# Optimization experiments

Hardware: AMD Instinct MI355X
Metric: run time of the kernel (lower is better)

## Reference

```python
import jax, jax.numpy as jnp
import numpy as np

LN_EPS = 1e-12


def setup_inputs() -> dict:
    key = jax.random.key(0)
    k1, k2, k3, k4 = jax.random.split(key, 4)
    B, H, L, D = 2, 12, 2048, 64
    q = jax.random.normal(k1, (B, H, L, D), dtype=jnp.float32)
    k = jax.random.normal(k2, (B, H, L, D), dtype=jnp.float32)
    v = jax.random.normal(k3, (B, H, L, D), dtype=jnp.float32)
    mask = jax.random.randint(k4, (1, 1, L, L), 0, 2).astype(jnp.int32)
    gamma = jnp.ones((D,), dtype=jnp.float32)
    beta = jnp.zeros((D,), dtype=jnp.float32)
    return {"q": q, "k": k, "v": v, "mask": mask, "gamma": gamma, "beta": beta}


def reference(q, k, v, mask, gamma, beta):
    # score = q @ k^T  -> [B, H, L, L]
    score = jnp.einsum("bhqd,bhkd->bhqk", q, k)
    # masked_fill(mask == 0, -10000)
    score = jnp.where(mask == 0, jnp.float32(-10000.0), score)
    # result = score @ v -> [B, H, L, D]  (no softmax)
    result = jnp.einsum("bhqk,bhkd->bhqd", score, v)
    # layer norm over the last dim (d_tensor)
    mean = jnp.mean(result, axis=-1, keepdims=True)
    var = jnp.var(result, axis=-1, keepdims=True)
    normed = (result - mean) / jnp.sqrt(var + LN_EPS)
    return normed * gamma + beta
```

## Files before the change

### kernel.cpp

```cpp
#include <hip/hip_runtime.h>

#define SEQ 2048
#define HD 64
#define NBH 24

#define MB_OFF   0
#define MB_BYTES (32 * 32 * 512)
#define QB_OFF   (MB_OFF + MB_BYTES)
#define QK_BYTES (NBH * SEQ * HD * 2)
#define KB_OFF   (QB_OFF + QK_BYTES)
#define VT_OFF   (KB_OFF + QK_BYTES)
#define WS_NEED  ((size_t)(VT_OFF + QK_BYTES))

typedef __bf16 bfrag8 __attribute__((ext_vector_type(8)));
typedef __bf16 bf16x4 __attribute__((ext_vector_type(4)));
typedef float  floatx4 __attribute__((ext_vector_type(4)));
typedef float  floatx16 __attribute__((ext_vector_type(16)));

__device__ __forceinline__ floatx4 mfma_16x16x32(bfrag8 a, bfrag8 b, floatx4 c) {
    return __builtin_amdgcn_mfma_f32_16x16x32_bf16(a, b, c, 0, 0, 0);
}
__device__ __forceinline__ floatx16 mfma_32x32x16(bfrag8 a, bfrag8 b, floatx16 c) {
    return __builtin_amdgcn_mfma_f32_32x32x16_bf16(a, b, c, 0, 0, 0);
}
__device__ __forceinline__ void gld16(const unsigned char* g, unsigned char* l) {
    __builtin_amdgcn_global_load_lds(
        (const __attribute__((address_space(1))) unsigned int*)g,
        (__attribute__((address_space(3))) unsigned int*)l, 16, 0, 0);
}

__global__ __launch_bounds__(256)
void prep_kernel(const float* __restrict__ qp, const float* __restrict__ kp,
                 const float* __restrict__ vp, const int* __restrict__ maskp,
                 unsigned char* __restrict__ ws)
{
    __shared__ __attribute__((aligned(16))) unsigned char parena[64 * 68 * 4];
    const int t = threadIdx.x;
    const int b = blockIdx.x;

    if (b < 1536) {
        int gt  = b * 256 + t;
        int row = gt >> 3;
        int c   = gt & 7;
        const floatx4* qs = (const floatx4*)(qp + row * 64 + c * 8);
        const floatx4* ks = (const floatx4*)(kp + row * 64 + c * 8);
        floatx4 q0 = qs[0], q1 = qs[1];
        floatx4 k0 = ks[0], k1 = ks[1];
        bfrag8 qpk, kpk;
        #pragma unroll
        for (int i = 0; i < 4; ++i) {
            qpk[i] = (__bf16)q0[i]; qpk[4 + i] = (__bf16)q1[i];
            kpk[i] = (__bf16)k0[i]; kpk[4 + i] = (__bf16)k1[i];
        }
        *(bfrag8*)(ws + QB_OFF + row * 128 + c * 16) = qpk;
        *(bfrag8*)(ws + KB_OFF + row * 128 + ((c ^ (row & 7)) * 16)) = kpk;
    } else if (b < 2304) {
        int bb = b - 1536, bh = bb >> 5, kt = bb & 31;
        float* lf = (float*)parena;
        const floatx4* vg = (const floatx4*)(vp + (bh * SEQ + kt * 64) * 64);
        #pragma unroll
        for (int it = 0; it < 4; ++it) {
            int f = t + it * 256;
            int r = f >> 4, c4 = f & 15;
            floatx4 val = vg[f];
            #pragma unroll
            for (int i = 0; i < 4; ++i) lf[r * 68 + c4 * 4 + i] = val[i];
        }
        __syncthreads();
        int d = t >> 2, kseg = t & 3;
        unsigned char* tb = ws + VT_OFF + (size_t)(bh * 32 + kt) * 8192 + d * 128;
        #pragma unroll
        for (int jj = 0; jj < 2; ++jj) {
            bfrag8 pk;
            #pragma unroll
            for (int e = 0; e < 8; ++e)
                pk[e] = (__bf16)lf[(kseg * 16 + jj * 8 + e) * 68 + d];
            *(bfrag8*)(tb + (((kseg * 2 + jj) ^ (d & 7)) * 16)) = pk;
        }
    } else {
        int cc = b - 2304, qtb = cc >> 5, kt = cc & 31;
        const int w = t >> 6, lane = t & 63;
        #pragma unroll
        for (int it = 0; it < 16; ++it) {
            int rr = it * 4 + w;
            unsigned long long bl = __ballot(maskp[(qtb * 64 + rr) * SEQ + kt * 64 + lane] != 0);
            if (lane == 0)
                *(unsigned long long*)(ws + MB_OFF + (size_t)((qtb * 32 + kt) * 64 + rr) * 8) = bl;
        }
    }
}

__global__ __launch_bounds__(128, 2)
void normattn_main(const unsigned char* __restrict__ ws,
                   const float* __restrict__ gammap, const float* __restrict__ betap,
                   float* __restrict__ outp)
{
    __shared__ __attribute__((aligned(16))) unsigned char sm[32768];

    const int tid  = threadIdx.x;
    const int w    = tid >> 6;
    const int lane = tid & 63;
    const int l32  = lane & 31;
    const int hi   = lane >> 5;

    const int id   = blockIdx.x;
    const int xcd  = id & 7;
    const int s    = id >> 3;
    const int bh   = xcd * 3 + (s >> 5);
    const int qtb  = s & 31;
    const int q0   = qtb * 64;

    unsigned char* slotK = sm + w * 16384;
    unsigned char* slotV = slotK + 8192;

    const unsigned char* gKt = ws + KB_OFF + (size_t)(bh * SEQ) * 128;
    const unsigned char* gVt = ws + VT_OFF + (size_t)(bh * 32) * 8192;
    const unsigned char* gMb = ws + MB_OFF + (size_t)(qtb * 32) * 512;

    bfrag8 qb[2][4];
    #pragma unroll
    for (int qh = 0; qh < 2; ++qh)
        #pragma unroll
        for (int dstep = 0; dstep < 4; ++dstep)
            qb[qh][dstep] = *(const bfrag8*)(ws + QB_OFF +
                (size_t)(bh * SEQ + q0 + qh * 32 + l32) * 128 + dstep * 32 + hi * 16);

    floatx16 acc[2][2];
    #pragma unroll
    for (int i = 0; i < 4; ++i) acc[i >> 1][i & 1] = (floatx16)0.0f;

    auto stage = [&](int kt) {
        const unsigned char* gk = gKt + (size_t)kt * 8192 + lane * 16;
        const unsigned char* gv = gVt + (size_t)kt * 8192 + lane * 16;
        #pragma unroll
        for (int c = 0; c < 8; ++c) {
            gld16(gk + c * 1024, slotK + c * 1024);
            gld16(gv + c * 1024, slotV + c * 1024);
        }
    };
    unsigned long long mnx0, mnx1;
    auto loadmask = [&](int kt) {
        mnx0 = *(const unsigned long long*)(gMb + (size_t)kt * 512 + l32 * 8);
        mnx1 = *(const unsigned long long*)(gMb + (size_t)kt * 512 + 256 + l32 * 8);
    };

    stage(w);
    loadmask(w);

    for (int i = 0; i < 16; ++i) {
        const int kt = w + 2 * i;
        asm volatile("s_waitcnt vmcnt(0)" ::: "memory");
        const unsigned long long mr0 = mnx0, mr1 = mnx1;

        bfrag8 ka[2][4], va[2][2][2];
        #pragma unroll
        for (int kh = 0; kh < 2; ++kh)
            #pragma unroll
            for (int d = 0; d < 4; ++d)
                ka[kh][d] = *(const bfrag8*)(slotK + (kh * 32 + l32) * 128 +
                                             (((d * 2 + hi) ^ (l32 & 7)) << 4));
        #pragma unroll
        for (int dh = 0; dh < 2; ++dh)
            #pragma unroll
            for (int kh = 0; kh < 2; ++kh)
                #pragma unroll
                for (int ks = 0; ks < 2; ++ks)
                    va[dh][kh][ks] = *(const bfrag8*)(slotV + (dh * 32 + l32) * 128 +
                                                      (((kh * 4 + ks * 2 + hi) ^ (l32 & 7)) << 4));
        asm volatile("s_waitcnt lgkmcnt(0)" ::: "memory");
        if (i < 15) { stage(kt + 2); loadmask(kt + 2); }

        #pragma unroll
        for (int kh = 0; kh < 2; ++kh) {
            floatx16 st0 = (floatx16)0.0f, st1 = (floatx16)0.0f;
            #pragma unroll
            for (int d = 0; d < 4; ++d) {
                st0 = mfma_32x32x16(ka[kh][d], qb[0][d], st0);
                st1 = mfma_32x32x16(ka[kh][d], qb[1][d], st1);
            }
            #pragma unroll
            for (int qh = 0; qh < 2; ++qh) {
                const floatx16 st = qh ? st1 : st0;
                const unsigned long long mrow = qh ? mr1 : mr0;
                const unsigned bits = (unsigned)(mrow >> (kh * 32 + 4 * hi));
                unsigned u[8];
                #pragma unroll
                for (int j = 0; j < 8; ++j) {
                    const int kl0 = 2 * (j & 1) + 8 * (j >> 1);
                    float a = ((bits >> kl0) & 1u) ? st[2 * j] : -10000.0f;
                    float b = ((bits >> (kl0 + 1)) & 1u) ? st[2 * j + 1] : -10000.0f;
                    asm("v_cvt_pk_bf16_f32 %0, %1, %2" : "=v"(u[j]) : "v"(a), "v"(b));
                }
                asm("v_permlane32_swap_b32 %0, %1" : "+v"(u[0]), "+v"(u[2]));
                asm("v_permlane32_swap_b32 %0, %1" : "+v"(u[1]), "+v"(u[3]));
                asm("v_permlane32_swap_b32 %0, %1" : "+v"(u[4]), "+v"(u[6]));
                asm("v_permlane32_swap_b32 %0, %1" : "+v"(u[5]), "+v"(u[7]));
                union { unsigned int w4[4]; bfrag8 f; } c0, c1;
                c0.w4[0] = u[0]; c0.w4[1] = u[1]; c0.w4[2] = u[2]; c0.w4[3] = u[3];
                c1.w4[0] = u[4]; c1.w4[1] = u[5]; c1.w4[2] = u[6]; c1.w4[3] = u[7];

                acc[qh][0] = mfma_32x32x16(va[0][kh][0], c0.f, acc[qh][0]);
                acc[qh][0] = mfma_32x32x16(va[0][kh][1], c1.f, acc[qh][0]);
                acc[qh][1] = mfma_32x32x16(va[1][kh][0], c0.f, acc[qh][1]);
                acc[qh][1] = mfma_32x32x16(va[1][kh][1], c1.f, acc[qh][1]);
            }
        }
    }

    unsigned char* ex = sm + 16384;
    if (w == 1) {
        #pragma unroll
        for (int qh = 0; qh < 2; ++qh)
            #pragma unroll
            for (int dh = 0; dh < 2; ++dh)
                #pragma unroll
                for (int jj = 0; jj < 4; ++jj) {
                    floatx4 t;
                    #pragma unroll
                    for (int e = 0; e < 4; ++e) t[e] = acc[qh][dh][jj * 4 + e];
                    *(floatx4*)(ex + (qh * 2 + dh) * 4096 + jj * 1024 + lane * 16) = t;
                }
    }
    __syncthreads();
    if (w == 0) {
        #pragma unroll
        for (int qh = 0; qh < 2; ++qh)
            #pragma unroll
            for (int dh = 0; dh < 2; ++dh)
                #pragma unroll
                for (int jj = 0; jj < 4; ++jj) {
                    floatx4 t = *(const floatx4*)(ex + (qh * 2 + dh) * 4096 + jj * 1024 + lane * 16);
                    #pragma unroll
                    for (int e = 0; e < 4; ++e) acc[qh][dh][jj * 4 + e] += t[e];
                }
        #pragma unroll
        for (int qh = 0; qh < 2; ++qh) {
            float ss = 0.0f, ss2 = 0.0f;
            #pragma unroll
            for (int dh = 0; dh < 2; ++dh)
                #pragma unroll
                for (int r = 0; r < 16; ++r) { float x = acc[qh][dh][r]; ss += x; ss2 += x * x; }
            ss  += __shfl_xor(ss, 32);
            ss2 += __shfl_xor(ss2, 32);
            float mean = ss * (1.0f / 64.0f);
            float var  = ss2 * (1.0f / 64.0f) - mean * mean;
            float rstd = rsqrtf(var + 1e-12f);
            float* orow = outp + (size_t)(bh * SEQ + q0 + qh * 32 + l32) * 64;
            #pragma unroll
            for (int dh = 0; dh < 2; ++dh)
                #pragma unroll
                for (int jj = 0; jj < 4; ++jj) {
                    const int d0 = dh * 32 + jj * 8 + 4 * hi;
                    floatx4 gg = *(const floatx4*)(gammap + d0);
                    floatx4 bb = *(const floatx4*)(betap + d0);
                    floatx4 o;
                    #pragma unroll
                    for (int e = 0; e < 4; ++e)
                        o[e] = (acc[qh][dh][jj * 4 + e] - mean) * rstd * gg[e] + bb[e];
                    *(floatx4*)(orow + d0) = o;
                }
        }
    }
}

#define KROW 72
#define SROW 40
__global__ __launch_bounds__(256, 4)
void normattn_fallback(const float* __restrict__ qp, const float* __restrict__ kp,
                       const float* __restrict__ vp, const int* __restrict__ maskp,
                       const float* __restrict__ gammap, const float* __restrict__ betap,
                       float* __restrict__ outp)
{
    __shared__ __attribute__((aligned(16))) __bf16 sQ[64 * KROW];
    __shared__ __attribute__((aligned(16))) __bf16 sK[64 * KROW];
    __shared__ __attribute__((aligned(16))) __bf16 sV[64 * KROW];
    __shared__ __attribute__((aligned(16))) __bf16 sS[4][16 * SROW];
    __shared__ __attribute__((aligned(8)))  unsigned int sMw[64][2];

    const int tid = threadIdx.x, wave = tid >> 6, lane = tid & 63;
    const int quad = lane >> 4, l16 = lane & 15;
    const int q0 = blockIdx.x * 64, bh = blockIdx.y;
    const int base = bh * SEQ * HD;
    {
        const floatx4* qg = (const floatx4*)(qp + base + q0 * HD);
        #pragma unroll
        for (int it = 0; it < 4; ++it) {
            int idx = tid + it * 256, r = idx >> 4, c = idx & 15;
            floatx4 val = qg[idx];
            bf16x4 pk = {(__bf16)val[0], (__bf16)val[1], (__bf16)val[2], (__bf16)val[3]};
            *(bf16x4*)&sQ[r * KROW + c * 4] = pk;
        }
    }
    __syncthreads();
    bfrag8 qa0 = *(const bfrag8*)&sQ[(wave * 16 + l16) * KROW + quad * 8];
    bfrag8 qa1 = *(const bfrag8*)&sQ[(wave * 16 + l16) * KROW + quad * 8 + 32];
    floatx4 acc[4];
    #pragma unroll
    for (int i = 0; i < 4; ++i) acc[i] = (floatx4)0.0f;
    const int qrow_loc = wave * 16 + quad * 4;
    const int qrb = q0 + qrow_loc;
    for (int kb = 0; kb < SEQ; kb += 64) {
        __syncthreads();
        {
            const floatx4* kg = (const floatx4*)(kp + base + kb * HD);
            #pragma unroll
            for (int it = 0; it < 4; ++it) {
                int idx = tid + it * 256, r = idx >> 4, c = idx & 15;
                floatx4 val = kg[idx];
                bf16x4 pk = {(__bf16)val[0], (__bf16)val[1], (__bf16)val[2], (__bf16)val[3]};
                *(bf16x4*)&sK[r * KROW + c * 4] = pk;
            }
        }
        {
            int d = tid & 63;
            #pragma unroll
            for (int it = 0; it < 4; ++it) {
                int k4 = (tid >> 6) + it * 4;
                bf16x4 pk;
                #pragma unroll
                for (int i = 0; i < 4; ++i) pk[i] = (__bf16)vp[base + (kb + k4 * 4 + i) * HD + d];
                *(bf16x4*)&sV[d * KROW + k4 * 4] = pk;
            }
        }
        #pragma unroll
        for (int it = 0; it < 16; ++it) {
            int rr = it * 4 + wave;
            unsigned long long bl = __ballot(maskp[(q0 + rr) * SEQ + kb + lane] != 0);
            if (lane == 0) { sMw[rr][0] = (unsigned)bl; sMw[rr][1] = (unsigned)(bl >> 32); }
        }
        __syncthreads();
        unsigned long long mrow[4];
        #pragma unroll
        for (int r = 0; r < 4; ++r) mrow[r] = *(const unsigned long long*)&sMw[qrow_loc + r][0];
        #pragma unroll
        for (int kc = 0; kc < 64; kc += 32) {
            floatx4 s0 = (floatx4)0.0f, s1 = (floatx4)0.0f;
            bfrag8 b00 = *(const bfrag8*)&sK[(kc + l16) * KROW + quad * 8];
            bfrag8 b01 = *(const bfrag8*)&sK[(kc + l16) * KROW + quad * 8 + 32];
            bfrag8 b10 = *(const bfrag8*)&sK[(kc + 16 + l16) * KROW + quad * 8];
            bfrag8 b11 = *(const bfrag8*)&sK[(kc + 16 + l16) * KROW + quad * 8 + 32];
            s0 = mfma_16x16x32(qa0, b00, s0);
            s0 = mfma_16x16x32(qa1, b01, s0);
            s1 = mfma_16x16x32(qa0, b10, s1);
            s1 = mfma_16x16x32(qa1, b11, s1);
            #pragma unroll
            for (int r = 0; r < 4; ++r) {
                float v0 = ((mrow[r] >> (kc + l16)) & 1ull) ? s0[r] : -10000.0f;
                float v1 = ((mrow[r] >> (kc + 16 + l16)) & 1ull) ? s1[r] : -10000.0f;
                sS[wave][(quad * 4 + r) * SROW + l16] = (__bf16)v0;
                sS[wave][(quad * 4 + r) * SROW + 16 + l16] = (__bf16)v1;
            }
            asm volatile("s_waitcnt lgkmcnt(0)" ::: "memory");
            bfrag8 pa = *(const bfrag8*)&sS[wave][l16 * SROW + quad * 8];
            #pragma unroll
            for (int nt = 0; nt < 4; ++nt) {
                bfrag8 vb = *(const bfrag8*)&sV[(nt * 16 + l16) * KROW + kc + quad * 8];
                acc[nt] = mfma_16x16x32(pa, vb, acc[nt]);
            }
        }
    }
    float g[4], bt[4];
    #pragma unroll
    for (int nt = 0; nt < 4; ++nt) { g[nt] = gammap[nt * 16 + l16]; bt[nt] = betap[nt * 16 + l16]; }
    #pragma unroll
    for (int r = 0; r < 4; ++r) {
        float s = 0.0f, s2 = 0.0f;
        #pragma unroll
        for (int nt = 0; nt < 4; ++nt) { float xx = acc[nt][r]; s += xx; s2 += xx * xx; }
        #pragma unroll
        for (int off = 1; off < 16; off <<= 1) { s += __shfl_xor(s, off); s2 += __shfl_xor(s2, off); }
        float mean = s * (1.0f / 64.0f);
        float var = s2 * (1.0f / 64.0f) - mean * mean;
        float rstd = rsqrtf(var + 1e-12f);
        float* orow = outp + base + (qrb + r) * HD;
        #pragma unroll
        for (int nt = 0; nt < 4; ++nt)
            orow[nt * 16 + l16] = (acc[nt][r] - mean) * rstd * g[nt] + bt[nt];
    }
}

extern "C" void kernel_launch(void* const* d_in, const int* in_sizes, int n_in,
                              void* d_out, int out_size, void* d_ws, size_t ws_size,
                              hipStream_t stream) {
    const float* q     = (const float*)d_in[0];
    const float* k     = (const float*)d_in[1];
    const float* v     = (const float*)d_in[2];
    const int*   mask  = (const int*)d_in[3];
    const float* gamma = (const float*)d_in[4];
    const float* beta  = (const float*)d_in[5];
    float* out = (float*)d_out;

    if (ws_size >= WS_NEED) {
        unsigned char* ws = (unsigned char*)d_ws;
        prep_kernel<<<3328, 256, 0, stream>>>(q, k, v, mask, ws);
        normattn_main<<<768, 128, 0, stream>>>(ws, gamma, beta, out);
    } else {
        dim3 grid(32, NBH);
        normattn_fallback<<<grid, 256, 0, stream>>>(q, k, v, mask, gamma, beta, out);
    }
}
```

Before: 141.9 us.

## Use single-wave blocks with double-buffered K/V tiles instead of two-wave split

Each block now runs one wave that processes all key tiles sequentially, using two LDS slots so the next tile's K/V and mask loads overlap compute. This removes the cross-wave accumulator reduction through LDS and the block barrier. In exchange, each block has half as many waves, so there is less parallelism per CU. Latency hiding now depends on the partial vmcnt waits.

```diff
diff --git a/kernel.cpp b/kernel.cpp
--- a/kernel.cpp
+++ b/kernel.cpp
@@ -90,16 +90,14 @@
     }
 }
 
-__global__ __launch_bounds__(128, 2)
+__global__ __launch_bounds__(64, 1)
 void normattn_main(const unsigned char* __restrict__ ws,
                    const float* __restrict__ gammap, const float* __restrict__ betap,
                    float* __restrict__ outp)
 {
     __shared__ __attribute__((aligned(16))) unsigned char sm[32768];
 
-    const int tid  = threadIdx.x;
-    const int w    = tid >> 6;
-    const int lane = tid & 63;
+    const int lane = threadIdx.x & 63;
     const int l32  = lane & 31;
     const int hi   = lane >> 5;
 
@@ -110,8 +108,8 @@
     const int qtb  = s & 31;
     const int q0   = qtb * 64;
 
-    unsigned char* slotK = sm + w * 16384;
-    unsigned char* slotV = slotK + 8192;
+    unsigned char* slotA = sm;
+    unsigned char* slotB = sm + 16384;
 
     const unsigned char* gKt = ws + KB_OFF + (size_t)(bh * SEQ) * 128;
     const unsigned char* gVt = ws + VT_OFF + (size_t)(bh * 32) * 8192;
@@ -129,30 +127,28 @@
     #pragma unroll
     for (int i = 0; i < 4; ++i) acc[i >> 1][i & 1] = (floatx16)0.0f;
 
-    auto stage = [&](int kt) {
+    auto stage = [&](int kt, unsigned char* slotK) {
         const unsigned char* gk = gKt + (size_t)kt * 8192 + lane * 16;
         const unsigned char* gv = gVt + (size_t)kt * 8192 + lane * 16;
+        unsigned char* slotV = slotK + 8192;
         #pragma unroll
         for (int c = 0; c < 8; ++c) {
             gld16(gk + c * 1024, slotK + c * 1024);
             gld16(gv + c * 1024, slotV + c * 1024);
         }
     };
-    unsigned long long mnx0, mnx1;
-    auto loadmask = [&](int kt) {
-        mnx0 = *(const unsigned long long*)(gMb + (size_t)kt * 512 + l32 * 8);
-        mnx1 = *(const unsigned long long*)(gMb + (size_t)kt * 512 + 256 + l32 * 8);
-    };
-
-    stage(w);
-    loadmask(w);
-
-    for (int i = 0; i < 16; ++i) {
-        const int kt = w + 2 * i;
-        asm volatile("s_waitcnt vmcnt(0)" ::: "memory");
-        const unsigned long long mr0 = mnx0, mr1 = mnx1;
-
-        bfrag8 ka[2][4], va[2][2][2];
+    unsigned long long mA0, mA1, mB0, mB1;
+    auto loadA = [&](int kt) {
+        mA0 = *(const unsigned long long*)(gMb + (size_t)kt * 512 + l32 * 8);
+        mA1 = *(const unsigned long long*)(gMb + (size_t)kt * 512 + 256 + l32 * 8);
+    };
+    auto loadB = [&](int kt) {
+        mB0 = *(const unsigned long long*)(gMb + (size_t)kt * 512 + l32 * 8);
+        mB1 = *(const unsigned long long*)(gMb + (size_t)kt * 512 + 256 + l32 * 8);
+    };
+
+    auto read_frags = [&](const unsigned char* slotK, bfrag8 (&ka)[2][4], bfrag8 (&va)[2][2][2]) {
+        const unsigned char* slotV = slotK + 8192;
         #pragma unroll
         for (int kh = 0; kh < 2; ++kh)
             #pragma unroll
@@ -167,9 +163,10 @@
                 for (int ks = 0; ks < 2; ++ks)
                     va[dh][kh][ks] = *(const bfrag8*)(slotV + (dh * 32 + l32) * 128 +
                                                       (((kh * 4 + ks * 2 + hi) ^ (l32 & 7)) << 4));
-        asm volatile("s_waitcnt lgkmcnt(0)" ::: "memory");
-        if (i < 15) { stage(kt + 2); loadmask(kt + 2); }
-
+    };
+
+    auto compute = [&](const bfrag8 (&ka)[2][4], const bfrag8 (&va)[2][2][2],
+                       unsigned long long mr0, unsigned long long mr1) {
         #pragma unroll
         for (int kh = 0; kh < 2; ++kh) {
             floatx16 st0 = (floatx16)0.0f, st1 = (floatx16)0.0f;
@@ -205,61 +202,59 @@
                 acc[qh][1] = mfma_32x32x16(va[1][kh][1], c1.f, acc[qh][1]);
             }
         }
-    }
-
-    unsigned char* ex = sm + 16384;
-    if (w == 1) {
-        #pragma unroll
-        for (int qh = 0; qh < 2; ++qh)
-            #pragma unroll
-            for (int dh = 0; dh < 2; ++dh)
+    };
+
+    stage(0, slotA); loadA(0);
+    stage(1, slotB); loadB(1);
+
+    for (int i = 0; i < 16; ++i) {
+        {
+            asm volatile("s_waitcnt vmcnt(18)" ::: "memory");
+            const unsigned long long m0 = mA0, m1 = mA1;
+            bfrag8 ka[2][4], va[2][2][2];
+            read_frags(slotA, ka, va);
+            asm volatile("s_waitcnt lgkmcnt(0)" ::: "memory");
+            if (i < 15) { stage(2 * i + 2, slotA); loadA(2 * i + 2); }
+            compute(ka, va, m0, m1);
+        }
+        {
+            if (i < 15) { asm volatile("s_waitcnt vmcnt(18)" ::: "memory"); }
+            else        { asm volatile("s_waitcnt vmcnt(0)"  ::: "memory"); }
+            const unsigned long long m0 = mB0, m1 = mB1;
+            bfrag8 ka[2][4], va[2][2][2];
+            read_frags(slotB, ka, va);
+            asm volatile("s_waitcnt lgkmcnt(0)" ::: "memory");
+            if (i < 15) { stage(2 * i + 3, slotB); loadB(2 * i + 3); }
+            compute(ka, va, m0, m1);
+        }
+    }
+
+    #pragma unroll
+    for (int qh = 0; qh < 2; ++qh) {
+        float ss = 0.0f, ss2 = 0.0f;
+        #pragma unroll
+        for (int dh = 0; dh < 2; ++dh)
+            #pragma unroll
+            for (int r = 0; r < 16; ++r) { float x = acc[qh][dh][r]; ss += x; ss2 += x * x; }
+        ss  += __shfl_xor(ss, 32);
+        ss2 += __shfl_xor(ss2, 32);
+        float mean = ss * (1.0f / 64.0f);
+        float var  = ss2 * (1.0f / 64.0f) - mean * mean;
+        float rstd = rsqrtf(var + 1e-12f);
+        float* orow = outp + (size_t)(bh * SEQ + q0 + qh * 32 + l32) * 64;
+        #pragma unroll
+        for (int dh = 0; dh < 2; ++dh)
+            #pragma unroll
+            for (int jj = 0; jj < 4; ++jj) {
+                const int d0 = dh * 32 + jj * 8 + 4 * hi;
+                floatx4 gg = *(const floatx4*)(gammap + d0);
+                floatx4 bb = *(const floatx4*)(betap + d0);
+                floatx4 o;
                 #pragma unroll
-                for (int jj = 0; jj < 4; ++jj) {
-                    floatx4 t;
-                    #pragma unroll
-                    for (int e = 0; e < 4; ++e) t[e] = acc[qh][dh][jj * 4 + e];
-                    *(floatx4*)(ex + (qh * 2 + dh) * 4096 + jj * 1024 + lane * 16) = t;
-                }
-    }
-    __syncthreads();
-    if (w == 0) {
-        #pragma unroll
-        for (int qh = 0; qh < 2; ++qh)
-            #pragma unroll
-            for (int dh = 0; dh < 2; ++dh)
-                #pragma unroll
-                for (int jj = 0; jj < 4; ++jj) {
-                    floatx4 t = *(const floatx4*)(ex + (qh * 2 + dh) * 4096 + jj * 1024 + lane * 16);
-                    #pragma unroll
-                    for (int e = 0; e < 4; ++e) acc[qh][dh][jj * 4 + e] += t[e];
-                }
-        #pragma unroll
-        for (int qh = 0; qh < 2; ++qh) {
-            float ss = 0.0f, ss2 = 0.0f;
-            #pragma unroll
-            for (int dh = 0; dh < 2; ++dh)
-                #pragma unroll
-                for (int r = 0; r < 16; ++r) { float x = acc[qh][dh][r]; ss += x; ss2 += x * x; }
-            ss  += __shfl_xor(ss, 32);
-            ss2 += __shfl_xor(ss2, 32);
-            float mean = ss * (1.0f / 64.0f);
-            float var  = ss2 * (1.0f / 64.0f) - mean * mean;
-            float rstd = rsqrtf(var + 1e-12f);
-            float* orow = outp + (size_t)(bh * SEQ + q0 + qh * 32 + l32) * 64;
-            #pragma unroll
-            for (int dh = 0; dh < 2; ++dh)
-                #pragma unroll
-                for (int jj = 0; jj < 4; ++jj) {
-                    const int d0 = dh * 32 + jj * 8 + 4 * hi;
-                    floatx4 gg = *(const floatx4*)(gammap + d0);
-                    floatx4 bb = *(const floatx4*)(betap + d0);
-                    floatx4 o;
-                    #pragma unroll
-                    for (int e = 0; e < 4; ++e)
-                        o[e] = (acc[qh][dh][jj * 4 + e] - mean) * rstd * gg[e] + bb[e];
-                    *(floatx4*)(orow + d0) = o;
-                }
-        }
+                for (int e = 0; e < 4; ++e)
+                    o[e] = (acc[qh][dh][jj * 4 + e] - mean) * rstd * gg[e] + bb[e];
+                *(floatx4*)(orow + d0) = o;
+            }
     }
 }
 
@@ -393,7 +388,7 @@
     if (ws_size >= WS_NEED) {
         unsigned char* ws = (unsigned char*)d_ws;
         prep_kernel<<<3328, 256, 0, stream>>>(q, k, v, mask, ws);
-        normattn_main<<<768, 128, 0, stream>>>(ws, gamma, beta, out);
+        normattn_main<<<768, 64, 0, stream>>>(ws, gamma, beta, out);
     } else {
         dim3 grid(32, NBH);
         normattn_fallback<<<grid, 256, 0, stream>>>(q, k, v, mask, gamma, beta, out);
```

After: 146.8 us. 3.5% more time.
